# Performance work log

Measured on AMD Instinct MI355X. Metric: run time of the kernel, lower is better.

## Reference

```python
import jax, jax.numpy as jnp
import numpy as np

# Geometry constants (from init_kwargs)
B, A, D = 16, 720, 1024          # batch, n_projections, n_detector_pixels
H, W = 512, 512                  # reconstruction volume
VOL_SPACING = 1.0                # pixel spacing (world units)
DET_SPACING = 1.0                # detector pixel spacing
ANG_RANGE = np.pi                # 180 deg parallel beam


def setup_inputs() -> dict:
    key = jax.random.key(0)
    sinogram = jax.random.normal(key, (B, A, D), dtype=jnp.float32)
    # Ramp (Ram-Lak) filter in FFT domain: |f| (real-valued), length D.
    freqs = np.fft.fftfreq(D)
    filt = jnp.asarray(2.0 * np.abs(freqs), dtype=jnp.float32)
    return {"sinogram": sinogram, "filt": filt}


def reference(sinogram, filt):
    # --- FFT ramp filtering along detector axis (norm='ortho') ---
    x = jnp.fft.fft(sinogram, axis=-1, norm="ortho")
    x = x * filt                                   # complex * real broadcast over [B,A,D]
    x = jnp.fft.ifft(x, axis=-1, norm="ortho").real.astype(jnp.float32)

    # --- Parallel-beam backprojection onto [H,W] grid ---
    angles = jnp.linspace(0.0, ANG_RANGE, A, endpoint=False, dtype=jnp.float32)
    cs, sn = jnp.cos(angles), jnp.sin(angles)      # [A]
    px = (jnp.arange(W, dtype=jnp.float32) - (W - 1) / 2.0) * VOL_SPACING  # [W]
    py = (jnp.arange(H, dtype=jnp.float32) - (H - 1) / 2.0) * VOL_SPACING  # [H]
    px = px[None, :]                               # [1,W]
    py = py[:, None]                               # [H,1]
    det_center = (D - 1) / 2.0

    sino_t = jnp.transpose(x, (1, 0, 2))           # [A,B,D]

    def step(acc, inp):
        c, s, proj = inp                           # proj: [B,D]
        # detector coordinate of each pixel's ray for this angle
        t = (px * c + py * s) / DET_SPACING + det_center   # [H,W]
        i0 = jnp.floor(t)
        w = t - i0                                 # linear-interp weight
        i0i = i0.astype(jnp.int32)
        i1i = i0i + 1
        valid = (i0i >= 0) & (i1i <= D - 1)
        i0c = jnp.clip(i0i, 0, D - 1)
        i1c = jnp.clip(i1i, 0, D - 1)
        v = proj[:, i0c] * (1.0 - w) + proj[:, i1c] * w    # [B,H,W]
        return acc + jnp.where(valid, v, 0.0), None

    img0 = jnp.zeros((B, H, W), dtype=jnp.float32)
    img, _ = jax.lax.scan(step, img0, (cs, sn, sino_t))
    # angular integration weight (d_theta = pi / A)
    return img * jnp.float32(ANG_RANGE / A)
```

## Files before the change

kernel.cpp:

```cpp
#include <hip/hip_runtime.h>
#include <hip/hip_fp16.h>
#include <math.h>

#define NB 16
#define NA 720
#define ND 1024
#define NH 512
#define NW 512

#define TW 32
#define TH 8
#define NBT 8
#define WINN 36

typedef __fp16 h2vec __attribute__((ext_vector_type(2)));

__device__ __forceinline__ uint32_t pkrtz_u32(float a, float b) {
    union { h2vec h; uint32_t u; } v;
    v.h = __builtin_amdgcn_cvt_pkrtz(a, b);
    return v.u;
}
__device__ __forceinline__ __half2 u32_to_h2(uint32_t u) {
    union { uint32_t u; __half2 h; } v; v.u = u; return v.h;
}
__device__ __forceinline__ uint32_t h2_to_u32(__half2 h) {
    union { __half2 h; uint32_t u; } v; v.h = h; return v.u;
}

__global__ __launch_bounds__(768) void prep_kernel(float4* __restrict__ ptable,
                                                   float2* __restrict__ twg) {
    const int a = threadIdx.x;
    const int pos = blockIdx.x;
    if (pos == 1024) {
        float ang = (float)(-2.0 * M_PI / 1024.0) * (float)a;
        float s, c;
        sincosf(ang, &s, &c);
        twg[a] = make_float2(c, s);
        return;
    }
    if (a >= NA) return;
    const float step = (float)(M_PI / (double)NA);
    float s, c;
    sincosf((float)a * step, &s, &c);
    const int bx = pos & 15, by = pos >> 4;
    const float x0 = (float)(bx * TW) - 255.5f;
    const float x1 = x0 + (float)(TW - 1);
    const float y0 = (float)(by * TH) - 255.5f;
    const float tmin = 511.5f + fminf(x0 * c, x1 * c) + y0 * s;
    const int base = (int)floorf(tmin) - 1;
    ptable[pos * NA + a] = make_float4(c, s, 511.5f - (float)base,
                                       __int_as_float(a * ND + base));
}

#define SZ(i) ((i) ^ (((i) >> 4) & 15))

__device__ __forceinline__ float2 cmul(float2 w, float2 v) {
    return make_float2(w.x * v.x - w.y * v.y, w.x * v.y + w.y * v.x);
}
__device__ __forceinline__ float2 cmulc(float2 w, float2 v) {
    return make_float2(w.x * v.x + w.y * v.y, w.x * v.y - w.y * v.x);
}

__global__ __launch_bounds__(256) void filter_kernel(const float* __restrict__ sino,
                                                     const float* __restrict__ filt,
                                                     const float2* __restrict__ twg,
                                                     uint32_t* __restrict__ packed) {
    __shared__ float2 bufA[ND];
    __shared__ float2 bufB[ND];
    __shared__ float2 tw4[768];

    const int tid = threadIdx.x;
    const int a = blockIdx.x;
    const int p = blockIdx.y;
    const float* __restrict__ xa = sino + ((size_t)(2 * p) * NA + a) * ND;
    const float* __restrict__ xb = xa + (size_t)NA * ND;
    uint32_t* __restrict__ yo = packed + ((size_t)(2 * p) * NA + a) * ND;

    #pragma unroll
    for (int i = 0; i < ND; i += 256)
        bufA[SZ(i + tid)] = make_float2(xa[i + tid], xb[i + tid]);
    #pragma unroll
    for (int i = 0; i < 768; i += 256) {
        int m = i + tid;
        tw4[SZ(m)] = twg[m];
    }
    __syncthreads();

    float2* src = bufA;
    float2* dst = bufB;

    for (int Ns = 1; Ns < ND; Ns <<= 2) {
        const int j = tid;
        const int m = j & (Ns - 1);
        const int tstep = (ND / 4) / Ns;
        float2 u0 = src[SZ(j)];
        float2 x1 = src[SZ(j + 256)];
        float2 x2 = src[SZ(j + 512)];
        float2 x3 = src[SZ(j + 768)];
        float2 w1 = tw4[SZ(m * tstep)];
        float2 w2 = tw4[SZ(2 * m * tstep)];
        float2 w3 = tw4[SZ(3 * m * tstep)];
        float2 u1 = cmul(w1, x1), u2 = cmul(w2, x2), u3 = cmul(w3, x3);
        float2 A  = make_float2(u0.x + u2.x, u0.y + u2.y);
        float2 Bb = make_float2(u0.x - u2.x, u0.y - u2.y);
        float2 C  = make_float2(u1.x + u3.x, u1.y + u3.y);
        float2 D  = make_float2(u1.x - u3.x, u1.y - u3.y);
        const int d = ((j & ~(Ns - 1)) << 2) + m;
        dst[SZ(d)]          = make_float2(A.x + C.x, A.y + C.y);
        dst[SZ(d + Ns)]     = make_float2(Bb.x + D.y, Bb.y - D.x);
        dst[SZ(d + 2 * Ns)] = make_float2(A.x - C.x, A.y - C.y);
        dst[SZ(d + 3 * Ns)] = make_float2(Bb.x - D.y, Bb.y + D.x);
        __syncthreads();
        float2* tmp = src; src = dst; dst = tmp;
    }

    const float SCALE = 1.0f / (float)ND;
    #pragma unroll
    for (int i = 0; i < ND; i += 256) {
        float f = filt[i + tid] * SCALE;
        src[SZ(i + tid)].x *= f;
        src[SZ(i + tid)].y *= f;
    }
    __syncthreads();

    for (int Ns = 1; Ns < ND; Ns <<= 2) {
        const int j = tid;
        const int m = j & (Ns - 1);
        const int tstep = (ND / 4) / Ns;
        float2 u0 = src[SZ(j)];
        float2 x1 = src[SZ(j + 256)];
        float2 x2 = src[SZ(j + 512)];
        float2 x3 = src[SZ(j + 768)];
        float2 w1 = tw4[SZ(m * tstep)];
        float2 w2 = tw4[SZ(2 * m * tstep)];
        float2 w3 = tw4[SZ(3 * m * tstep)];
        float2 u1 = cmulc(w1, x1), u2 = cmulc(w2, x2), u3 = cmulc(w3, x3);
        float2 A  = make_float2(u0.x + u2.x, u0.y + u2.y);
        float2 Bb = make_float2(u0.x - u2.x, u0.y - u2.y);
        float2 C  = make_float2(u1.x + u3.x, u1.y + u3.y);
        float2 D  = make_float2(u1.x - u3.x, u1.y - u3.y);
        const int d = ((j & ~(Ns - 1)) << 2) + m;
        dst[SZ(d)]          = make_float2(A.x + C.x, A.y + C.y);
        dst[SZ(d + Ns)]     = make_float2(Bb.x - D.y, Bb.y + D.x);
        dst[SZ(d + 2 * Ns)] = make_float2(A.x - C.x, A.y - C.y);
        dst[SZ(d + 3 * Ns)] = make_float2(Bb.x + D.y, Bb.y - D.x);
        __syncthreads();
        float2* tmp = src; src = dst; dst = tmp;
    }

    #pragma unroll
    for (int i = 0; i < ND; i += 256) {
        float2 v = src[SZ(i + tid)];
        yo[i + tid] = pkrtz_u32(v.x, v.y);
    }
}

__global__ __launch_bounds__(256, 8) void backproj_kernel(const uint32_t* __restrict__ packed,
                                                          const float4* __restrict__ ptable,
                                                          float* __restrict__ img) {
    __shared__ __align__(16) uint4 win[2][8][WINN];

    const int tid = threadIdx.x;
    const int bx = blockIdx.x, by = blockIdx.y, bz = blockIdx.z;

    const float4* __restrict__ pt = ptable + (size_t)((by << 4) + bx) * NA;

    const bool stg = tid < 2 * WINN;
    const int sg   = (tid >= WINN) ? 1 : 0;
    const int si   = tid - sg * WINN;
    const uint32_t* __restrict__ sbA =
        packed + (size_t)(2 * (4 * bz + 2 * sg)) * NA * ND + si;
    const uint32_t* __restrict__ sbB = sbA + (size_t)2 * NA * ND;
    uint4* const wptr = &win[sg][0][si];

    const int lane = tid & 63;
    const int wid  = tid >> 6;
    const int tx   = (wid << 3) + (lane & 7);
    const int ty   = lane >> 3;
    const float px  = (float)(bx * TW + tx) - 255.5f;
    const float pyf = (float)(by * TH + ty) - 255.5f;

    float accf[8];
    __half2 hacc01, hacc23, hacc45, hacc67;
    #pragma unroll
    for (int b = 0; b < 8; b++) accf[b] = 0.0f;
    hacc01 = u32_to_h2(0u); hacc23 = u32_to_h2(0u);
    hacc45 = u32_to_h2(0u); hacc67 = u32_to_h2(0u);

    auto bar = []() {
        asm volatile("s_waitcnt lgkmcnt(0)" ::: "memory");
        __builtin_amdgcn_s_barrier();
    };

    auto stage_load = [&](float4 P, uint2& wA, uint2& wB) {
        const int off = __float_as_int(P.w);
        const uint32_t* pa = sbA + off;
        const uint32_t* pb = sbB + off;
        wA = make_uint2(pa[0], pa[1]);
        wB = make_uint2(pb[0], pb[1]);
    };
    auto stage_write = [&](int ph, uint2 wA, uint2 wB) {
        wptr[ph * WINN] = make_uint4(
            wA.x, h2_to_u32(__hsub2(u32_to_h2(wA.y), u32_to_h2(wA.x))),
            wB.x, h2_to_u32(__hsub2(u32_to_h2(wB.y), u32_to_h2(wB.x))));
    };
    auto consume = [&](float4 P, int ph) {
        const float t = fmaf(px, P.x, fmaf(pyf, P.y, P.z));
        const int i0 = (int)t;
#if __has_builtin(__builtin_amdgcn_fractf)
        float w = __builtin_amdgcn_fractf(t);
#else
        float w = t - (float)i0;
#endif
        __half2 wh2 = u32_to_h2(pkrtz_u32(w, w));
        const uint4 qA = win[0][ph][i0];
        const uint4 qB = win[1][ph][i0];
        hacc01 = __hfma2(wh2, u32_to_h2(qA.y), __hadd2(hacc01, u32_to_h2(qA.x)));
        hacc23 = __hfma2(wh2, u32_to_h2(qA.w), __hadd2(hacc23, u32_to_h2(qA.z)));
        hacc45 = __hfma2(wh2, u32_to_h2(qB.y), __hadd2(hacc45, u32_to_h2(qB.x)));
        hacc67 = __hfma2(wh2, u32_to_h2(qB.w), __hadd2(hacc67, u32_to_h2(qB.z)));
    };

    uint2 h0A = make_uint2(0, 0), h0B = make_uint2(0, 0);
    uint2 h1A = make_uint2(0, 0), h1B = make_uint2(0, 0);
    uint2 h2A = make_uint2(0, 0), h2B = make_uint2(0, 0);
    uint2 h3A = make_uint2(0, 0), h3B = make_uint2(0, 0);

    if (stg) {
        uint2 wA, wB;
        stage_load(pt[0], wA, wB);  stage_write(0, wA, wB);
        stage_load(pt[1], wA, wB);  stage_write(1, wA, wB);
        stage_load(pt[2], wA, wB);  stage_write(2, wA, wB);
        stage_load(pt[3], wA, wB);  stage_write(3, wA, wB);
        stage_load(pt[4], h0A, h0B);
        stage_load(pt[5], h1A, h1B);
        stage_load(pt[6], h2A, h2B);
        stage_load(pt[7], h3A, h3B);
    }
    bar();

    #pragma unroll 1
    for (int r = 0; r < NA / 4; ++r) {
        const int a = 4 * r;
        const int cb = (r & 1) * 4;
        const int ob = cb ^ 4;
        const float4 P0 = pt[a],     P1 = pt[a + 1];
        const float4 P2 = pt[a + 2], P3 = pt[a + 3];

        if (stg) {
            stage_write(ob + 0, h0A, h0B);
            stage_write(ob + 1, h1A, h1B);
            stage_write(ob + 2, h2A, h2B);
            stage_write(ob + 3, h3A, h3B);
            stage_load(pt[min(a + 8,  NA - 1)], h0A, h0B);
            stage_load(pt[min(a + 9,  NA - 1)], h1A, h1B);
            stage_load(pt[min(a + 10, NA - 1)], h2A, h2B);
            stage_load(pt[min(a + 11, NA - 1)], h3A, h3B);
        }
        consume(P0, cb + 0);
        consume(P1, cb + 1);
        consume(P2, cb + 2);
        consume(P3, cb + 3);

        if ((r & 3) == 3) {
            float2 v01 = __half22float2(hacc01);
            float2 v23 = __half22float2(hacc23);
            float2 v45 = __half22float2(hacc45);
            float2 v67 = __half22float2(hacc67);
            accf[0] += v01.x; accf[1] += v01.y;
            accf[2] += v23.x; accf[3] += v23.y;
            accf[4] += v45.x; accf[5] += v45.y;
            accf[6] += v67.x; accf[7] += v67.y;
            hacc01 = u32_to_h2(0u); hacc23 = u32_to_h2(0u);
            hacc45 = u32_to_h2(0u); hacc67 = u32_to_h2(0u);
        }
        bar();
    }

    const float SCALE = (float)(M_PI / (double)NA);
    const size_t bstride = (size_t)NH * NW;
    size_t o0 = (((size_t)(bz * NBT) * NH) + (by * TH + ty)) * NW + (bx * TW + tx);
    #pragma unroll
    for (int b = 0; b < 8; b++)
        img[o0 + (size_t)b * bstride] = accf[b] * SCALE;
}

extern "C" void kernel_launch(void* const* d_in, const int* in_sizes, int n_in,
                              void* d_out, int out_size, void* d_ws, size_t ws_size,
                              hipStream_t stream) {
    const float* sino = (const float*)d_in[0];
    const float* filt = (const float*)d_in[1];
    float* out = (float*)d_out;

    const size_t pack_bytes = (size_t)NB * NA * ND * sizeof(uint32_t);
    const size_t ptab_bytes = (size_t)1024 * NA * sizeof(float4);
    const size_t twg_bytes  = (size_t)768 * sizeof(float2);

    uint32_t* packed;
    float4* ptable;
    float2* twg;

    if (ws_size >= pack_bytes + ptab_bytes + twg_bytes) {
        packed = (uint32_t*)d_ws;
        ptable = (float4*)((char*)d_ws + pack_bytes);
        twg    = (float2*)((char*)d_ws + pack_bytes + ptab_bytes);
    } else {
        packed = (uint32_t*)d_in[0];
        ptable = (float4*)d_ws;
        twg    = (float2*)((char*)d_ws + ptab_bytes);
    }

    prep_kernel<<<dim3(1025), dim3(768), 0, stream>>>(ptable, twg);
    filter_kernel<<<dim3(NA, NB / 2), dim3(256), 0, stream>>>(sino, filt, twg, packed);
    backproj_kernel<<<dim3(NW / TW, NH / TH, NB / NBT), dim3(256), 0, stream>>>(packed, ptable, out);
}
```

Baseline: 356.7 us.

## Precompute interleaved value/delta layout and stage windows via global_load_lds

The filter kernel now writes a batch-interleaved 16-byte record per detector bin, holding the fp16 value and the fp16 difference to the next bin, so the backprojector no longer computes deltas or packs data at staging time. The backprojection kernel uses direct global-to-LDS async loads, issued by one wavefront, to stage 64-entry windows for four angles at a time into double-buffered shared memory. This cuts staging instructions and barriers per angle. In exchange it writes a larger intermediate buffer, and the fallback path keeps the old kernel when the workspace is too small.

```diff
diff --git a/kernel.cpp b/kernel.cpp
--- a/kernel.cpp
+++ b/kernel.cpp
@@ -11,7 +11,7 @@
 #define TW 32
 #define TH 8
 #define NBT 8
-#define WINN 36
+#define WREG 64
 
 typedef __fp16 h2vec __attribute__((ext_vector_type(2)));
 
@@ -64,6 +64,7 @@
 __global__ __launch_bounds__(256) void filter_kernel(const float* __restrict__ sino,
                                                      const float* __restrict__ filt,
                                                      const float2* __restrict__ twg,
+                                                     uint4* __restrict__ gq,
                                                      uint32_t* __restrict__ packed) {
     __shared__ float2 bufA[ND];
     __shared__ float2 bufB[ND];
@@ -74,7 +75,6 @@
     const int p = blockIdx.y;
     const float* __restrict__ xa = sino + ((size_t)(2 * p) * NA + a) * ND;
     const float* __restrict__ xb = xa + (size_t)NA * ND;
-    uint32_t* __restrict__ yo = packed + ((size_t)(2 * p) * NA + a) * ND;
 
     #pragma unroll
     for (int i = 0; i < ND; i += 256)
@@ -148,16 +148,133 @@
         float2* tmp = src; src = dst; dst = tmp;
     }
 
-    #pragma unroll
-    for (int i = 0; i < ND; i += 256) {
-        float2 v = src[SZ(i + tid)];
-        yo[i + tid] = pkrtz_u32(v.x, v.y);
-    }
-}
-
-__global__ __launch_bounds__(256, 8) void backproj_kernel(const uint32_t* __restrict__ packed,
+    if (gq != nullptr) {
+        char* gb = (char*)(gq + ((size_t)(p >> 1) * NA + a) * ND) + (p & 1) * 8;
+        #pragma unroll
+        for (int i = 0; i < ND; i += 256) {
+            const int idx = i + tid;
+            float2 v = src[SZ(idx)];
+            uint32_t u = pkrtz_u32(v.x, v.y);
+            float2 vn = src[SZ(min(idx + 1, ND - 1))];
+            uint32_t un = pkrtz_u32(vn.x, vn.y);
+            *(uint2*)(gb + (size_t)idx * 16) = make_uint2(
+                u, h2_to_u32(__hsub2(u32_to_h2(un), u32_to_h2(u))));
+        }
+    } else {
+        uint32_t* __restrict__ yo = packed + ((size_t)(2 * p) * NA + a) * ND;
+        #pragma unroll
+        for (int i = 0; i < ND; i += 256) {
+            float2 v = src[SZ(i + tid)];
+            yo[i + tid] = pkrtz_u32(v.x, v.y);
+        }
+    }
+}
+
+__global__ __launch_bounds__(256, 8) void backproj_kernel(const uint4* __restrict__ gq,
                                                           const float4* __restrict__ ptable,
                                                           float* __restrict__ img) {
+    __shared__ __align__(16) uint4 win[2][4][2][WREG];
+
+    const int tid = threadIdx.x;
+    const int bx = blockIdx.x, by = blockIdx.y, bz = blockIdx.z;
+
+    const float4* __restrict__ pt = ptable + (size_t)((by << 4) + bx) * NA;
+
+    const int lane = tid & 63;
+    const int wid  = tid >> 6;
+    const int tx   = (wid << 3) + (lane & 7);
+    const int ty   = lane >> 3;
+    const float px  = (float)(bx * TW + tx) - 255.5f;
+    const float pyf = (float)(by * TH + ty) - 255.5f;
+
+    const uint4* __restrict__ q0 = gq + (size_t)(2 * bz) * NA * ND + lane;
+    const uint4* __restrict__ q1 = q0 + (size_t)NA * ND;
+
+    float accf[8];
+    __half2 hacc01 = u32_to_h2(0u), hacc23 = u32_to_h2(0u),
+            hacc45 = u32_to_h2(0u), hacc67 = u32_to_h2(0u);
+    #pragma unroll
+    for (int b = 0; b < 8; b++) accf[b] = 0.0f;
+
+    auto gld = [](const uint4* g, uint4* l) {
+        __builtin_amdgcn_global_load_lds(
+            (const __attribute__((address_space(1))) void*)g,
+            (__attribute__((address_space(3))) void*)l, 16, 0, 0);
+    };
+    auto stage4 = [&](int a, uint4* bank) {
+        #pragma unroll
+        for (int j = 0; j < 4; j++) {
+            const int off = __float_as_int(pt[min(a + j, NA - 1)].w);
+            gld(q0 + off, bank + j * (2 * WREG));
+            gld(q1 + off, bank + j * (2 * WREG) + WREG);
+        }
+    };
+    auto consume = [&](float4 P, const uint4* wb, int ph) {
+        const float t = fmaf(px, P.x, fmaf(pyf, P.y, P.z));
+        const int i0 = (int)t;
+#if __has_builtin(__builtin_amdgcn_fractf)
+        float w = __builtin_amdgcn_fractf(t);
+#else
+        float w = t - (float)i0;
+#endif
+        __half2 wh2 = u32_to_h2(pkrtz_u32(w, w));
+        const uint4 qA = wb[ph * 2 * WREG + i0];
+        const uint4 qB = wb[ph * 2 * WREG + WREG + i0];
+        hacc01 = __hfma2(wh2, u32_to_h2(qA.y), __hadd2(hacc01, u32_to_h2(qA.x)));
+        hacc23 = __hfma2(wh2, u32_to_h2(qA.w), __hadd2(hacc23, u32_to_h2(qA.z)));
+        hacc45 = __hfma2(wh2, u32_to_h2(qB.y), __hadd2(hacc45, u32_to_h2(qB.x)));
+        hacc67 = __hfma2(wh2, u32_to_h2(qB.w), __hadd2(hacc67, u32_to_h2(qB.z)));
+    };
+
+    if (wid == 0) {
+        stage4(0, &win[0][0][0][0]);
+        asm volatile("s_waitcnt vmcnt(0)" ::: "memory");
+    }
+    __builtin_amdgcn_s_barrier();
+
+    #pragma unroll 1
+    for (int r = 0; r < NA / 4; ++r) {
+        const int a = 4 * r;
+        const uint4* wb = &win[r & 1][0][0][0];
+        if (wid == 0)
+            stage4(a + 4, &win[(r + 1) & 1][0][0][0]);
+        const float4 P0 = pt[a],     P1 = pt[a + 1];
+        const float4 P2 = pt[a + 2], P3 = pt[a + 3];
+        consume(P0, wb, 0);
+        consume(P1, wb, 1);
+        consume(P2, wb, 2);
+        consume(P3, wb, 3);
+
+        if ((r & 3) == 3) {
+            float2 v01 = __half22float2(hacc01);
+            float2 v23 = __half22float2(hacc23);
+            float2 v45 = __half22float2(hacc45);
+            float2 v67 = __half22float2(hacc67);
+            accf[0] += v01.x; accf[1] += v01.y;
+            accf[2] += v23.x; accf[3] += v23.y;
+            accf[4] += v45.x; accf[5] += v45.y;
+            accf[6] += v67.x; accf[7] += v67.y;
+            hacc01 = u32_to_h2(0u); hacc23 = u32_to_h2(0u);
+            hacc45 = u32_to_h2(0u); hacc67 = u32_to_h2(0u);
+        }
+        if (wid == 0)
+            asm volatile("s_waitcnt vmcnt(0)" ::: "memory");
+        asm volatile("s_waitcnt lgkmcnt(0)" ::: "memory");
+        __builtin_amdgcn_s_barrier();
+    }
+
+    const float SCALE = (float)(M_PI / (double)NA);
+    const size_t bstride = (size_t)NH * NW;
+    size_t o0 = (((size_t)(bz * NBT) * NH) + (by * TH + ty)) * NW + (bx * TW + tx);
+    #pragma unroll
+    for (int b = 0; b < 8; b++)
+        img[o0 + (size_t)b * bstride] = accf[b] * SCALE;
+}
+
+#define WINN 36
+__global__ __launch_bounds__(256, 8) void backproj_fb(const uint32_t* __restrict__ packed,
+                                                      const float4* __restrict__ ptable,
+                                                      float* __restrict__ img) {
     __shared__ __align__(16) uint4 win[2][8][WINN];
 
     const int tid = threadIdx.x;
@@ -181,23 +298,19 @@
     const float pyf = (float)(by * TH + ty) - 255.5f;
 
     float accf[8];
-    __half2 hacc01, hacc23, hacc45, hacc67;
+    __half2 hacc01 = u32_to_h2(0u), hacc23 = u32_to_h2(0u),
+            hacc45 = u32_to_h2(0u), hacc67 = u32_to_h2(0u);
     #pragma unroll
     for (int b = 0; b < 8; b++) accf[b] = 0.0f;
-    hacc01 = u32_to_h2(0u); hacc23 = u32_to_h2(0u);
-    hacc45 = u32_to_h2(0u); hacc67 = u32_to_h2(0u);
 
     auto bar = []() {
         asm volatile("s_waitcnt lgkmcnt(0)" ::: "memory");
         __builtin_amdgcn_s_barrier();
     };
-
     auto stage_load = [&](float4 P, uint2& wA, uint2& wB) {
         const int off = __float_as_int(P.w);
-        const uint32_t* pa = sbA + off;
-        const uint32_t* pb = sbB + off;
-        wA = make_uint2(pa[0], pa[1]);
-        wB = make_uint2(pb[0], pb[1]);
+        wA = make_uint2(sbA[off], sbA[off + 1]);
+        wB = make_uint2(sbB[off], sbB[off + 1]);
     };
     auto stage_write = [&](int ph, uint2 wA, uint2 wB) {
         wptr[ph * WINN] = make_uint4(
@@ -292,25 +405,23 @@
     const float* filt = (const float*)d_in[1];
     float* out = (float*)d_out;
 
-    const size_t pack_bytes = (size_t)NB * NA * ND * sizeof(uint32_t);
+    const size_t gq_bytes   = (size_t)4 * NA * ND * sizeof(uint4);
     const size_t ptab_bytes = (size_t)1024 * NA * sizeof(float4);
     const size_t twg_bytes  = (size_t)768 * sizeof(float2);
 
-    uint32_t* packed;
-    float4* ptable;
-    float2* twg;
-
-    if (ws_size >= pack_bytes + ptab_bytes + twg_bytes) {
-        packed = (uint32_t*)d_ws;
-        ptable = (float4*)((char*)d_ws + pack_bytes);
-        twg    = (float2*)((char*)d_ws + pack_bytes + ptab_bytes);
+    if (ws_size >= gq_bytes + ptab_bytes + twg_bytes) {
+        uint4*  gq     = (uint4*)d_ws;
+        float4* ptable = (float4*)((char*)d_ws + gq_bytes);
+        float2* twg    = (float2*)((char*)d_ws + gq_bytes + ptab_bytes);
+        prep_kernel<<<dim3(1025), dim3(768), 0, stream>>>(ptable, twg);
+        filter_kernel<<<dim3(NA, NB / 2), dim3(256), 0, stream>>>(sino, filt, twg, gq, nullptr);
+        backproj_kernel<<<dim3(NW / TW, NH / TH, NB / NBT), dim3(256), 0, stream>>>(gq, ptable, out);
     } else {
-        packed = (uint32_t*)d_in[0];
-        ptable = (float4*)d_ws;
-        twg    = (float2*)((char*)d_ws + ptab_bytes);
-    }
-
-    prep_kernel<<<dim3(1025), dim3(768), 0, stream>>>(ptable, twg);
-    filter_kernel<<<dim3(NA, NB / 2), dim3(256), 0, stream>>>(sino, filt, twg, packed);
-    backproj_kernel<<<dim3(NW / TW, NH / TH, NB / NBT), dim3(256), 0, stream>>>(packed, ptable, out);
-}
+        uint32_t* packed = (uint32_t*)d_in[0];
+        float4* ptable   = (float4*)d_ws;
+        float2* twg      = (float2*)((char*)d_ws + ptab_bytes);
+        prep_kernel<<<dim3(1025), dim3(768), 0, stream>>>(ptable, twg);
+        filter_kernel<<<dim3(NA, NB / 2), dim3(256), 0, stream>>>(sino, filt, twg, nullptr, packed);
+        backproj_fb<<<dim3(NW / TW, NH / TH, NB / NBT), dim3(256), 0, stream>>>(packed, ptable, out);
+    }
+}
```

Result: faster. 342.0 us (-4.1%).
